# Performance work log

Hardware: AMD Instinct MI355X
Metric: run time of the kernel (lower is better)

The kernel has to match this reference:

```python
import jax, jax.numpy as jnp
import numpy as np

NUM_CLS = 80
C = 256
IMG = 1024.0
N = 256
SR = 2  # sampling_ratio
MIN_SIZE = 16.0
SCALES = (0.25, 0.125, 0.0625, 0.03125)
HW = ((256, 256), (128, 128), (64, 64), (32, 32))


def _roialign(feat, rois, scale, out):
    # feat: [C, H, W]; rois: [n, 4] (y1, x1, y2, x2) in image coords.
    # torchvision-style ROIAlign (aligned=False), sampling_ratio=SR, avg pool.
    Cc, H, W = feat.shape
    n = rois.shape[0]
    y1 = rois[:, 0] * scale
    x1 = rois[:, 1] * scale
    rh = jnp.maximum(rois[:, 2] * scale - y1, 1.0)
    rw = jnp.maximum(rois[:, 3] * scale - x1, 1.0)
    # per-bin sample offsets: (bin + (s+0.5)/SR) * bin_size
    g = (jnp.arange(out, dtype=feat.dtype)[:, None]
         + (jnp.arange(SR, dtype=feat.dtype)[None, :] + 0.5) / SR).reshape(-1)  # [out*SR]
    ys = y1[:, None] + g[None, :] * (rh / out)[:, None]  # [n, out*SR]
    xs = x1[:, None] + g[None, :] * (rw / out)[:, None]
    S = out * SR
    yy = jnp.broadcast_to(ys[:, :, None], (n, S, S)).reshape(n, S * S)
    xx = jnp.broadcast_to(xs[:, None, :], (n, S, S)).reshape(n, S * S)
    valid = (yy > -1.0) & (yy < H) & (xx > -1.0) & (xx < W)
    yc = jnp.clip(yy, 0.0, H - 1.0)
    xc = jnp.clip(xx, 0.0, W - 1.0)
    y0 = jnp.floor(yc)
    x0 = jnp.floor(xc)
    ly = yc - y0
    lx = xc - x0
    y0i = y0.astype(jnp.int32)
    x0i = x0.astype(jnp.int32)
    y1i = jnp.minimum(y0i + 1, H - 1)
    x1i = jnp.minimum(x0i + 1, W - 1)
    f00 = feat[:, y0i, x0i]  # [C, n, S*S]
    f01 = feat[:, y0i, x1i]
    f10 = feat[:, y1i, x0i]
    f11 = feat[:, y1i, x1i]
    val = (f00 * (1 - ly) * (1 - lx) + f01 * (1 - ly) * lx
           + f10 * ly * (1 - lx) + f11 * ly * lx)
    val = jnp.where(valid[None], val, 0.0)
    val = val.reshape(Cc, n, out, SR, out, SR).mean(axis=(3, 5))
    return val.transpose(1, 0, 2, 3)  # [n, C, out, out]


def _pool(P, rois, out):
    # roi_layer: FPN level assignment via log2 of sqrt(area)/224, clamp to levels 0..3
    area = jnp.prod(rois[:, 2:4] - rois[:, 0:2] + 1.0, axis=-1)
    lvl = jnp.clip(jnp.floor(4.0 + jnp.log(jnp.sqrt(area) / 224.0) / np.log(2.0)), 2.0, 5.0) - 2.0
    lvl = lvl.astype(jnp.int32)
    pooled = jnp.zeros((rois.shape[0], C, out, out), dtype=rois.dtype)
    for l in range(4):
        pl = _roialign(P[l], rois, SCALES[l], out)
        pooled = pooled + jnp.where((lvl == l)[:, None, None, None], pl, 0.0)
    return pooled


def _loc2bbox(loc, anchor):
    chw = anchor[..., 2:4] - anchor[..., 0:2]
    cyx = anchor[..., 0:2] + chw * 0.5
    yx = loc[..., 0:2] * chw + cyx
    hw = jnp.exp(loc[..., 2:4]) * chw
    return jnp.concatenate([yx - hw * 0.5, yx + hw * 0.5], axis=-1)


def _head(x, W1, b1, W2, b2, Wc, bc, Wl, bl):
    x = x.reshape(x.shape[0], -1)
    h = jax.nn.relu(x @ W1 + b1)
    h = jax.nn.relu(h @ W2 + b2)
    return h @ Wc + bc, h @ Wl + bl


def _cascade(P, rois, params):
    stds = (jnp.array([0.1, 0.1, 0.2, 0.2], dtype=rois.dtype),
            jnp.array([0.05, 0.05, 0.1, 0.1], dtype=rois.dtype),
            jnp.array([1 / 30.0, 1 / 30.0, 1 / 15.0, 1 / 15.0], dtype=rois.dtype))
    roi = rois
    valid = jnp.ones((rois.shape[0],), dtype=bool)
    t = jnp.arange(rois.shape[0])
    pre_b = jnp.zeros((rois.shape[0], NUM_CLS, 4), dtype=rois.dtype)
    pre_s = jnp.zeros((rois.shape[0], NUM_CLS), dtype=rois.dtype)
    for s in range(3):
        x = _pool(P, roi, 7)
        logits, loc = _head(x, *params[s])
        loc = loc.reshape(-1, NUM_CLS + 1, 4)[:, 1:] * stds[s]
        boxes = _loc2bbox(loc, roi[:, None, :])  # [N, NUM_CLS, 4]
        score = jax.nn.softmax(logits, axis=-1)[:, 1:]
        pre_b = pre_b + boxes
        pre_s = pre_s + score
        best = jnp.argmax(score, axis=-1)
        roi = boxes[t, best]
        roi = jnp.clip(roi, 0.0, IMG)  # square image: clamp both coords to [0, IMG]
        if s < 2:  # original filters only after stages 1 and 2
            hw = roi[:, 2:4] - roi[:, 0:2]
            valid = valid & jnp.all(hw >= MIN_SIZE, axis=-1)
    m = valid.astype(pre_s.dtype)
    return pre_b / 3.0 * m[:, None, None], pre_s / 3.0 * m[:, None]


def setup_inputs():
    key = jax.random.key(0)
    ks = jax.random.split(key, 32)
    inp = {}
    for i, (h, w) in enumerate(HW):
        inp[f"P{i}"] = jax.random.normal(ks[i], (C, h, w), dtype=jnp.float32)
    yx1 = jax.random.uniform(ks[4], (N, 2), minval=0.0, maxval=IMG - 64.0)
    sz = jnp.exp(jax.random.uniform(ks[5], (N, 2), minval=np.log(16.0), maxval=np.log(600.0)))
    yx2 = jnp.clip(yx1 + sz, 0.0, IMG - 1.0)
    inp["rois"] = jnp.concatenate([yx1, yx2], axis=-1).astype(jnp.float32)
    dims = [(C * 49, 1024), (1024,), (1024, 1024), (1024,),
            (1024, NUM_CLS + 1), (NUM_CLS + 1,), (1024, (NUM_CLS + 1) * 4), ((NUM_CLS + 1) * 4,)]
    names = ["W1", "b1", "W2", "b2", "Wc", "bc", "Wl", "bl"]
    k = 6
    for s in range(3):
        for nm, d in zip(names, dims):
            if len(d) == 1:
                inp[f"s{s}_{nm}"] = jnp.zeros(d, dtype=jnp.float32)
            else:
                inp[f"s{s}_{nm}"] = 0.02 * jax.random.normal(ks[k], d, dtype=jnp.float32)
                k += 1
    return inp


def reference(P0, P1, P2, P3, rois,
              s0_W1, s0_b1, s0_W2, s0_b2, s0_Wc, s0_bc, s0_Wl, s0_bl,
              s1_W1, s1_b1, s1_W2, s1_b2, s1_Wc, s1_bc, s1_Wl, s1_bl,
              s2_W1, s2_b1, s2_W2, s2_b2, s2_Wc, s2_bc, s2_Wl, s2_bl):
    P = (P0, P1, P2, P3)
    params = [(s0_W1, s0_b1, s0_W2, s0_b2, s0_Wc, s0_bc, s0_Wl, s0_bl),
              (s1_W1, s1_b1, s1_W2, s1_b2, s1_Wc, s1_bc, s1_Wl, s1_bl),
              (s2_W1, s2_b1, s2_W2, s2_b2, s2_Wc, s2_bc, s2_Wl, s2_bl)]
    return _cascade(P, rois, params)
```

## Files before the change

kernel.cpp:

```cpp
#include <hip/hip_runtime.h>
#include <math.h>


#define NROI 256
#define NCLS 80
#define APITCH 40

typedef __attribute__((ext_vector_type(8))) short short8;
typedef __attribute__((ext_vector_type(4))) float f32x4;

__device__ __forceinline__ unsigned short f2bf(float f) {
  unsigned u = __builtin_bit_cast(unsigned, f);
  unsigned r = (u + 0x7FFFu + ((u >> 16) & 1u)) >> 16;
  return (unsigned short)r;
}
__device__ __forceinline__ float bf2f(unsigned short u) {
  return __builtin_bit_cast(float, (unsigned)u << 16);
}

__global__ __launch_bounds__(256) void init_kernel(const float* __restrict__ rois,
                                                   float* __restrict__ roi,
                                                   float* __restrict__ valid) {
  int i = blockIdx.x * 256 + threadIdx.x;
  if (i < NROI * 4) roi[i] = rois[i];
  if (i < NROI) valid[i] = 1.0f;
}

__global__ __launch_bounds__(256) void transpose_bf16(const float* __restrict__ W,
                                                      unsigned short* __restrict__ Wt,
                                                      int K, int N) {
  __shared__ unsigned short tile[32][33];
  int t = threadIdx.x;
  int k0 = blockIdx.x * 32;
  int n0 = blockIdx.y * 32;
  int r = t >> 3;
  int c4 = (t & 7) * 4;
  float4 v = *(const float4*)(W + (size_t)(k0 + r) * N + n0 + c4);
  tile[r][c4 + 0] = f2bf(v.x);
  tile[r][c4 + 1] = f2bf(v.y);
  tile[r][c4 + 2] = f2bf(v.z);
  tile[r][c4 + 3] = f2bf(v.w);
  __syncthreads();
  struct __attribute__((aligned(8))) US4 { unsigned short a, b, c, d; } o;
  o.a = tile[c4 + 0][r];
  o.b = tile[c4 + 1][r];
  o.c = tile[c4 + 2][r];
  o.d = tile[c4 + 3][r];
  *(US4*)(Wt + (size_t)(n0 + r) * K + k0 + c4) = o;
}

__global__ __launch_bounds__(256) void transpose_w1(const float* __restrict__ W,
                                                    unsigned short* __restrict__ Wt) {
  __shared__ unsigned short tile[32][33];
  int t = threadIdx.x;
  int kd0 = blockIdx.x * 32;
  int n0 = blockIdx.y * 32;
  int p = kd0 >> 8;
  int c0 = kd0 & 255;
  int r = t >> 3;
  int c4 = (t & 7) * 4;
  int k_src = (c0 + r) * 49 + p;
  float4 v = *(const float4*)(W + (size_t)k_src * 1024 + n0 + c4);
  tile[r][c4 + 0] = f2bf(v.x);
  tile[r][c4 + 1] = f2bf(v.y);
  tile[r][c4 + 2] = f2bf(v.z);
  tile[r][c4 + 3] = f2bf(v.w);
  __syncthreads();
  struct __attribute__((aligned(8))) US4 { unsigned short a, b, c, d; } o;
  o.a = tile[c4 + 0][r];
  o.b = tile[c4 + 1][r];
  o.c = tile[c4 + 2][r];
  o.d = tile[c4 + 3][r];
  *(US4*)(Wt + (size_t)(n0 + r) * 12544 + kd0 + c4) = o;
}

__global__ __launch_bounds__(256) void head_transpose(const float* __restrict__ Wc,
                                                      const float* __restrict__ Wl,
                                                      unsigned short* __restrict__ Wt) {
  __shared__ unsigned short tile[32][33];
  int t = threadIdx.x;
  int k0 = blockIdx.x * 32;
  int n0 = blockIdx.y * 32;
  int r = t >> 3;
  int c4 = (t & 7) * 4;
#pragma unroll
  for (int j = 0; j < 4; j++) {
    int nn = n0 + c4 + j;
    float v = 0.0f;
    if (nn < 81) v = Wc[(size_t)(k0 + r) * 81 + nn];
    else if (nn < 405) v = Wl[(size_t)(k0 + r) * 324 + (nn - 81)];
    tile[r][c4 + j] = f2bf(v);
  }
  __syncthreads();
  struct __attribute__((aligned(8))) US4 { unsigned short a, b, c, d; } o;
  o.a = tile[c4 + 0][r];
  o.b = tile[c4 + 1][r];
  o.c = tile[c4 + 2][r];
  o.d = tile[c4 + 3][r];
  *(US4*)(Wt + (size_t)(n0 + r) * 1024 + k0 + c4) = o;
}

__global__ __launch_bounds__(256) void pool_kernel2(
    const unsigned short* __restrict__ Pb0, const unsigned short* __restrict__ Pb1,
    const unsigned short* __restrict__ Pb2, const unsigned short* __restrict__ Pb3,
    const float* __restrict__ roi, unsigned short* __restrict__ pooled) {
  int t = threadIdx.x;
  int n = blockIdx.y;
  int p = blockIdx.x * 4 + (t >> 6);
  if (p >= 49) return;
  int lane = t & 63;
  int c4 = lane * 4;
  int py = p / 7, px = p % 7;

  float r0 = roi[n * 4 + 0];
  float r1 = roi[n * 4 + 1];
  float r2 = roi[n * 4 + 2];
  float r3 = roi[n * 4 + 3];

  float area = (r2 - r0 + 1.0f) * (r3 - r1 + 1.0f);
  float lf = floorf(4.0f + log2f(sqrtf(area) / 224.0f));
  lf = fminf(fmaxf(lf, 2.0f), 5.0f);
  int lvl = (int)lf - 2;

  float scale;
  int H;
  const unsigned short* fb;
  if (lvl == 0)      { scale = 0.25f;    H = 256; fb = Pb0; }
  else if (lvl == 1) { scale = 0.125f;   H = 128; fb = Pb1; }
  else if (lvl == 2) { scale = 0.0625f;  H = 64;  fb = Pb2; }
  else               { scale = 0.03125f; H = 32;  fb = Pb3; }
  int W = H;

  float y1 = r0 * scale;
  float x1 = r1 * scale;
  float rh = fmaxf(r2 * scale - y1, 1.0f);
  float rw = fmaxf(r3 * scale - x1, 1.0f);
  float bh = rh * (1.0f / 7.0f);
  float bw = rw * (1.0f / 7.0f);

  float a0 = 0.f, a1 = 0.f, a2 = 0.f, a3 = 0.f;
#pragma unroll
  for (int ry = 0; ry < 2; ry++) {
    float yy = y1 + ((float)py + ((float)ry + 0.5f) * 0.5f) * bh;
    bool vy = (yy > -1.0f) && (yy < (float)H);
    float ycl = fminf(fmaxf(yy, 0.0f), (float)(H - 1));
    float y0f = floorf(ycl);
    float ly = ycl - y0f;
    int y0i = (int)y0f;
    int y1i = min(y0i + 1, H - 1);
#pragma unroll
    for (int rx = 0; rx < 2; rx++) {
      float xx = x1 + ((float)px + ((float)rx + 0.5f) * 0.5f) * bw;
      bool vx = (xx > -1.0f) && (xx < (float)W);
      float xcl = fminf(fmaxf(xx, 0.0f), (float)(W - 1));
      float x0f = floorf(xcl);
      float lx = xcl - x0f;
      int x0i = (int)x0f;
      int x1i = min(x0i + 1, W - 1);
      float w00 = (1.f - ly) * (1.f - lx);
      float w01 = (1.f - ly) * lx;
      float w10 = ly * (1.f - lx);
      float w11 = ly * lx;
      if (!(vy && vx)) { w00 = w01 = w10 = w11 = 0.f; }
      ushort4 f00 = *(const ushort4*)(fb + ((size_t)(y0i * W + x0i) * 256 + c4));
      ushort4 f01 = *(const ushort4*)(fb + ((size_t)(y0i * W + x1i) * 256 + c4));
      ushort4 f10 = *(const ushort4*)(fb + ((size_t)(y1i * W + x0i) * 256 + c4));
      ushort4 f11 = *(const ushort4*)(fb + ((size_t)(y1i * W + x1i) * 256 + c4));
      a0 += bf2f(f00.x) * w00 + bf2f(f01.x) * w01 + bf2f(f10.x) * w10 + bf2f(f11.x) * w11;
      a1 += bf2f(f00.y) * w00 + bf2f(f01.y) * w01 + bf2f(f10.y) * w10 + bf2f(f11.y) * w11;
      a2 += bf2f(f00.z) * w00 + bf2f(f01.z) * w01 + bf2f(f10.z) * w10 + bf2f(f11.z) * w11;
      a3 += bf2f(f00.w) * w00 + bf2f(f01.w) * w01 + bf2f(f10.w) * w10 + bf2f(f11.w) * w11;
    }
  }
  ushort4 o;
  o.x = f2bf(a0 * 0.25f);
  o.y = f2bf(a1 * 0.25f);
  o.z = f2bf(a2 * 0.25f);
  o.w = f2bf(a3 * 0.25f);
  *(ushort4*)(pooled + (size_t)n * 12544 + p * 256 + c4) = o;
}

__global__ __launch_bounds__(256) void gemm_bf16(
    const unsigned short* __restrict__ A, const unsigned short* __restrict__ B,
    float* __restrict__ Cpart, int M, int N, int K, int iters) {
  __shared__ unsigned short As[128 * APITCH];
  __shared__ unsigned short Bs[128 * APITCH];
  const int t = threadIdx.x;
  const int n0 = blockIdx.x * 128;
  const int m0 = blockIdx.y * 128;
  const size_t kt0 = (size_t)blockIdx.z * iters * 32;

  const int row = t >> 2;
  const int off = (t & 3) * 8;
  const unsigned short* pa0 = A + (size_t)(m0 + row) * K + kt0 + off;
  const unsigned short* pa1 = pa0 + (size_t)64 * K;
  const unsigned short* pb0 = B + (size_t)(n0 + row) * K + kt0 + off;
  const unsigned short* pb1 = pb0 + (size_t)64 * K;

  const int lane = t & 63;
  const int wave = t >> 6;
  const int wm = (wave >> 1) * 64;
  const int wn = (wave & 1) * 64;
  const int fr = lane & 15;
  const int kq = (lane >> 4) * 8;

  f32x4 acc[4][4];
#pragma unroll
  for (int i = 0; i < 4; i++)
#pragma unroll
    for (int j = 0; j < 4; j++) acc[i][j] = (f32x4){0.f, 0.f, 0.f, 0.f};

  uint4 ra0 = *(const uint4*)pa0;
  uint4 ra1 = *(const uint4*)pa1;
  uint4 rb0 = *(const uint4*)pb0;
  uint4 rb1 = *(const uint4*)pb1;

  for (int it = 0; it < iters; ++it) {
    *(uint4*)&As[row * APITCH + off] = ra0;
    *(uint4*)&As[(row + 64) * APITCH + off] = ra1;
    *(uint4*)&Bs[row * APITCH + off] = rb0;
    *(uint4*)&Bs[(row + 64) * APITCH + off] = rb1;
    __syncthreads();
    if (it + 1 < iters) {
      int d = (it + 1) * 32;
      ra0 = *(const uint4*)(pa0 + d);
      ra1 = *(const uint4*)(pa1 + d);
      rb0 = *(const uint4*)(pb0 + d);
      rb1 = *(const uint4*)(pb1 + d);
    }
    short8 af[4], bfv[4];
#pragma unroll
    for (int f = 0; f < 4; f++)
      af[f] = *(const short8*)&As[(wm + f * 16 + fr) * APITCH + kq];
#pragma unroll
    for (int f = 0; f < 4; f++)
      bfv[f] = *(const short8*)&Bs[(wn + f * 16 + fr) * APITCH + kq];
#pragma unroll
    for (int fm = 0; fm < 4; fm++)
#pragma unroll
      for (int fn = 0; fn < 4; fn++)
        acc[fm][fn] = __builtin_amdgcn_mfma_f32_16x16x32_bf16(af[fm], bfv[fn],
                                                              acc[fm][fn], 0, 0, 0);
    __syncthreads();
  }

  float* Cp = Cpart + (size_t)blockIdx.z * M * N;
  const int colb = n0 + wn + fr;
  const int rowb = m0 + wm + (lane >> 4) * 4;
#pragma unroll
  for (int fm = 0; fm < 4; fm++)
#pragma unroll
    for (int fn = 0; fn < 4; fn++)
#pragma unroll
      for (int r = 0; r < 4; r++)
        Cp[(size_t)(rowb + fm * 16 + r) * N + (colb + fn * 16)] = acc[fm][fn][r];
}

__global__ __launch_bounds__(256) void reduce_bias_relu(
    const float* __restrict__ parts, int nparts, const float* __restrict__ bias,
    unsigned short* __restrict__ outb) {
  int i = blockIdx.x * 256 + threadIdx.x;
  float s = 0.0f;
  for (int p = 0; p < nparts; ++p) s += parts[(size_t)p * 262144 + i];
  s = fmaxf(s + bias[i & 1023], 0.0f);
  outb[i] = f2bf(s);
}

__global__ __launch_bounds__(128) void decode_kernel(
    const float* __restrict__ headp, const float* __restrict__ bc,
    const float* __restrict__ bl,
    float* __restrict__ roi, float* __restrict__ valid,
    float* __restrict__ pre_b, float* __restrict__ pre_s,
    float st0, float st1, float st2, float st3, int stage) {
  int n = blockIdx.x;
  int t = threadIdx.x;
  __shared__ float red[128];
  __shared__ int redi[128];
  __shared__ float sroi[4];
  __shared__ float boxes[NCLS][4];

  if (t < 4) sroi[t] = roi[n * 4 + t];
  float l = -INFINITY;
  if (t < 81) {
    float s = 0.f;
#pragma unroll
    for (int z = 0; z < 4; z++) s += headp[(size_t)z * 131072 + n * 512 + t];
    l = s + bc[t];
  }
  red[t] = l;
  __syncthreads();
#pragma unroll
  for (int s = 64; s > 0; s >>= 1) {
    if (t < s) red[t] = fmaxf(red[t], red[t + s]);
    __syncthreads();
  }
  float mx = red[0];
  __syncthreads();
  red[t] = (t < 81) ? expf(l - mx) : 0.0f;
  __syncthreads();
#pragma unroll
  for (int s = 64; s > 0; s >>= 1) {
    if (t < s) red[t] += red[t + s];
    __syncthreads();
  }
  float denom = red[0];
  __syncthreads();

  float score = -INFINITY;
  if (t < NCLS) {
    float lj = 0.f;
#pragma unroll
    for (int z = 0; z < 4; z++) lj += headp[(size_t)z * 131072 + n * 512 + (t + 1)];
    lj += bc[t + 1];
    score = expf(lj - mx) / denom;
    float lp[4];
#pragma unroll
    for (int j = 0; j < 4; j++) {
      float s = 0.f;
#pragma unroll
      for (int z = 0; z < 4; z++)
        s += headp[(size_t)z * 131072 + n * 512 + 81 + (t + 1) * 4 + j];
      lp[j] = s + bl[(t + 1) * 4 + j];
    }
    float dy = lp[0] * st0;
    float dx = lp[1] * st1;
    float dh = lp[2] * st2;
    float dw = lp[3] * st3;
    float h_ = sroi[2] - sroi[0];
    float w_ = sroi[3] - sroi[1];
    float cy = sroi[0] + h_ * 0.5f;
    float cx = sroi[1] + w_ * 0.5f;
    float ny = dy * h_ + cy;
    float nx = dx * w_ + cx;
    float nh = expf(dh) * h_;
    float nw = expf(dw) * w_;
    float b0 = ny - nh * 0.5f;
    float b1v = nx - nw * 0.5f;
    float b2v = ny + nh * 0.5f;
    float b3v = nx + nw * 0.5f;
    int o = (n * NCLS + t) * 4;
    pre_b[o + 0] += b0;
    pre_b[o + 1] += b1v;
    pre_b[o + 2] += b2v;
    pre_b[o + 3] += b3v;
    pre_s[n * NCLS + t] += score;
    boxes[t][0] = b0;
    boxes[t][1] = b1v;
    boxes[t][2] = b2v;
    boxes[t][3] = b3v;
  }
  red[t] = score;
  redi[t] = t;
  __syncthreads();
  for (int s = 64; s > 0; s >>= 1) {
    if (t < s) {
      float o2 = red[t + s];
      int oi = redi[t + s];
      if (o2 > red[t] || (o2 == red[t] && oi < redi[t])) {
        red[t] = o2;
        redi[t] = oi;
      }
    }
    __syncthreads();
  }
  if (t == 0) {
    int best = redi[0];
    float ry1 = fminf(fmaxf(boxes[best][0], 0.0f), 1024.0f);
    float rx1 = fminf(fmaxf(boxes[best][1], 0.0f), 1024.0f);
    float ry2 = fminf(fmaxf(boxes[best][2], 0.0f), 1024.0f);
    float rx2 = fminf(fmaxf(boxes[best][3], 0.0f), 1024.0f);
    roi[n * 4 + 0] = ry1;
    roi[n * 4 + 1] = rx1;
    roi[n * 4 + 2] = ry2;
    roi[n * 4 + 3] = rx2;
    if (stage < 2) {
      float hh = ry2 - ry1, ww = rx2 - rx1;
      if (!(hh >= 16.0f && ww >= 16.0f)) valid[n] = 0.0f;
    }
  }
}

__global__ __launch_bounds__(256) void finalize_kernel(
    const float* __restrict__ pre_b, const float* __restrict__ pre_s,
    const float* __restrict__ valid, float* __restrict__ out) {
  int i = blockIdx.x * 256 + threadIdx.x;
  if (i < NROI * NCLS * 4) {
    int n = i / (NCLS * 4);
    out[i] = pre_b[i] * valid[n] * (1.0f / 3.0f);
  } else if (i < NROI * NCLS * 4 + NROI * NCLS) {
    int j = i - NROI * NCLS * 4;
    int n = j / NCLS;
    out[i] = pre_s[j] * valid[n] * (1.0f / 3.0f);
  }
}

extern "C" void kernel_launch(void* const* d_in, const int* in_sizes, int n_in,
                              void* d_out, int out_size, void* d_ws, size_t ws_size,
                              hipStream_t stream) {
  const float* P0 = (const float*)d_in[0];
  const float* P1 = (const float*)d_in[1];
  const float* P2 = (const float*)d_in[2];
  const float* P3 = (const float*)d_in[3];
  const float* rois = (const float*)d_in[4];
  float* out = (float*)d_out;
  float* ws = (float*)d_ws;

  float* roi   = ws;
  float* valid = roi + 1024;
  float* pre_b = valid + 256;
  float* pre_s = pre_b + 81920;
  float* part1 = pre_s + 20480;
  float* part2 = part1 + 14 * 262144;
  float* parth = part2 + 8 * 262144;
  unsigned short* pooledb = (unsigned short*)(parth + 4 * 131072);
  unsigned short* Wt1 = pooledb + (size_t)256 * 12544;
  unsigned short* Wt2 = Wt1 + (size_t)1024 * 12544;
  unsigned short* Wth = Wt2 + (size_t)1024 * 1024;
  unsigned short* h1b = Wth + (size_t)512 * 1024;
  unsigned short* h2b = h1b + (size_t)256 * 1024;
  unsigned short* Pb0 = h2b + (size_t)256 * 1024;
  unsigned short* Pb1 = Pb0 + (size_t)65536 * 256;
  unsigned short* Pb2 = Pb1 + (size_t)16384 * 256;
  unsigned short* Pb3 = Pb2 + (size_t)4096 * 256;

  init_kernel<<<4, 256, 0, stream>>>(rois, roi, valid);
  hipMemsetAsync(pre_b, 0, (size_t)(81920 + 20480) * sizeof(float), stream);

  transpose_bf16<<<dim3(8, 2048), 256, 0, stream>>>(P0, Pb0, 256, 65536);
  transpose_bf16<<<dim3(8, 512),  256, 0, stream>>>(P1, Pb1, 256, 16384);
  transpose_bf16<<<dim3(8, 128),  256, 0, stream>>>(P2, Pb2, 256, 4096);
  transpose_bf16<<<dim3(8, 32),   256, 0, stream>>>(P3, Pb3, 256, 1024);

  const float stds[3][4] = {
      {0.1f, 0.1f, 0.2f, 0.2f},
      {0.05f, 0.05f, 0.1f, 0.1f},
      {1.0f / 30.0f, 1.0f / 30.0f, 1.0f / 15.0f, 1.0f / 15.0f}};

  for (int s = 0; s < 3; s++) {
    const float* W1 = (const float*)d_in[5 + s * 8 + 0];
    const float* b1 = (const float*)d_in[5 + s * 8 + 1];
    const float* W2 = (const float*)d_in[5 + s * 8 + 2];
    const float* b2 = (const float*)d_in[5 + s * 8 + 3];
    const float* Wc = (const float*)d_in[5 + s * 8 + 4];
    const float* bc = (const float*)d_in[5 + s * 8 + 5];
    const float* Wl = (const float*)d_in[5 + s * 8 + 6];
    const float* bl = (const float*)d_in[5 + s * 8 + 7];

    transpose_w1<<<dim3(392, 32), 256, 0, stream>>>(W1, Wt1);
    transpose_bf16<<<dim3(32, 32), 256, 0, stream>>>(W2, Wt2, 1024, 1024);
    head_transpose<<<dim3(32, 16), 256, 0, stream>>>(Wc, Wl, Wth);

    pool_kernel2<<<dim3(13, 256), 256, 0, stream>>>(Pb0, Pb1, Pb2, Pb3, roi, pooledb);

    gemm_bf16<<<dim3(8, 2, 14), 256, 0, stream>>>(pooledb, Wt1, part1, 256, 1024, 12544, 28);
    reduce_bias_relu<<<1024, 256, 0, stream>>>(part1, 14, b1, h1b);

    gemm_bf16<<<dim3(8, 2, 8), 256, 0, stream>>>(h1b, Wt2, part2, 256, 1024, 1024, 4);
    reduce_bias_relu<<<1024, 256, 0, stream>>>(part2, 8, b2, h2b);

    gemm_bf16<<<dim3(4, 2, 4), 256, 0, stream>>>(h2b, Wth, parth, 256, 512, 1024, 8);

    decode_kernel<<<256, 128, 0, stream>>>(parth, bc, bl, roi, valid, pre_b, pre_s,
                                           stds[s][0], stds[s][1], stds[s][2], stds[s][3], s);
  }

  finalize_kernel<<<400, 256, 0, stream>>>(pre_b, pre_s, valid, out);
}
```

Baseline: 499.5 us.

## Merge all feature and weight conversions into one prep launch, fold init/finalize into decode

```diff
diff --git a/kernel.cpp b/kernel.cpp
--- a/kernel.cpp
+++ b/kernel.cpp
@@ -18,24 +18,85 @@
   return __builtin_bit_cast(float, (unsigned)u << 16);
 }
 
-__global__ __launch_bounds__(256) void init_kernel(const float* __restrict__ rois,
-                                                   float* __restrict__ roi,
-                                                   float* __restrict__ valid) {
-  int i = blockIdx.x * 256 + threadIdx.x;
-  if (i < NROI * 4) roi[i] = rois[i];
-  if (i < NROI) valid[i] = 1.0f;
-}
-
-__global__ __launch_bounds__(256) void transpose_bf16(const float* __restrict__ W,
-                                                      unsigned short* __restrict__ Wt,
-                                                      int K, int N) {
+__global__ __launch_bounds__(256) void prep_kernel(
+    const float* __restrict__ P0, const float* __restrict__ P1,
+    const float* __restrict__ P2, const float* __restrict__ P3,
+    unsigned short* __restrict__ Pb0, unsigned short* __restrict__ Pb1,
+    unsigned short* __restrict__ Pb2, unsigned short* __restrict__ Pb3,
+    const float* __restrict__ W1a, const float* __restrict__ W1b,
+    const float* __restrict__ W1c,
+    const float* __restrict__ W2a, const float* __restrict__ W2b,
+    const float* __restrict__ W2c,
+    const float* __restrict__ Wca, const float* __restrict__ Wcb,
+    const float* __restrict__ Wcc,
+    const float* __restrict__ Wla, const float* __restrict__ Wlb,
+    const float* __restrict__ Wlc,
+    unsigned short* __restrict__ Wt1, unsigned short* __restrict__ Wt2,
+    unsigned short* __restrict__ Wth) {
   __shared__ unsigned short tile[32][33];
+  int bid = blockIdx.x;
   int t = threadIdx.x;
-  int k0 = blockIdx.x * 32;
-  int n0 = blockIdx.y * 32;
   int r = t >> 3;
   int c4 = (t & 7) * 4;
-  float4 v = *(const float4*)(W + (size_t)(k0 + r) * N + n0 + c4);
+
+  float4 v;
+  unsigned short* dptr;
+
+  if (bid < 21760) {
+    const float* S;
+    unsigned short* D;
+    int N, idx;
+    if (bid < 16384)      { S = P0; D = Pb0; N = 65536; idx = bid; }
+    else if (bid < 20480) { S = P1; D = Pb1; N = 16384; idx = bid - 16384; }
+    else if (bid < 21504) { S = P2; D = Pb2; N = 4096;  idx = bid - 20480; }
+    else                  { S = P3; D = Pb3; N = 1024;  idx = bid - 21504; }
+    int k0 = (idx & 7) * 32;
+    int n0 = (idx >> 3) * 32;
+    v = *(const float4*)(S + (size_t)(k0 + r) * N + n0 + c4);
+    dptr = D + (size_t)(n0 + r) * 256 + k0 + c4;
+  } else if (bid < 59392) {
+    int idx = bid - 21760;
+    int s = idx / 12544;
+    idx -= s * 12544;
+    const float* W = (s == 0) ? W1a : (s == 1) ? W1b : W1c;
+    int bx = idx % 392;
+    int by = idx / 392;
+    int kd0 = bx * 32;
+    int n0 = by * 32;
+    int p = kd0 >> 8;
+    int c0 = kd0 & 255;
+    v = *(const float4*)(W + (size_t)((c0 + r) * 49 + p) * 1024 + n0 + c4);
+    dptr = Wt1 + (size_t)s * 12544 * 1024 + (size_t)(n0 + r) * 12544 + kd0 + c4;
+  } else if (bid < 62464) {
+    int idx = bid - 59392;
+    int s = idx >> 10;
+    idx &= 1023;
+    const float* W = (s == 0) ? W2a : (s == 1) ? W2b : W2c;
+    int k0 = (idx & 31) * 32;
+    int n0 = (idx >> 5) * 32;
+    v = *(const float4*)(W + (size_t)(k0 + r) * 1024 + n0 + c4);
+    dptr = Wt2 + (size_t)s * 1024 * 1024 + (size_t)(n0 + r) * 1024 + k0 + c4;
+  } else {
+    int idx = bid - 62464;
+    int s = idx >> 9;
+    idx &= 511;
+    const float* wc = (s == 0) ? Wca : (s == 1) ? Wcb : Wcc;
+    const float* wl = (s == 0) ? Wla : (s == 1) ? Wlb : Wlc;
+    int k0 = (idx & 31) * 32;
+    int n0 = (idx >> 5) * 32;
+    float vv[4];
+#pragma unroll
+    for (int j = 0; j < 4; j++) {
+      int nn = n0 + c4 + j;
+      float x = 0.0f;
+      if (nn < 81) x = wc[(size_t)(k0 + r) * 81 + nn];
+      else if (nn < 405) x = wl[(size_t)(k0 + r) * 324 + (nn - 81)];
+      vv[j] = x;
+    }
+    v.x = vv[0]; v.y = vv[1]; v.z = vv[2]; v.w = vv[3];
+    dptr = Wth + (size_t)s * 512 * 1024 + (size_t)(n0 + r) * 1024 + k0 + c4;
+  }
+
   tile[r][c4 + 0] = f2bf(v.x);
   tile[r][c4 + 1] = f2bf(v.y);
   tile[r][c4 + 2] = f2bf(v.z);
@@ -46,58 +107,7 @@
   o.b = tile[c4 + 1][r];
   o.c = tile[c4 + 2][r];
   o.d = tile[c4 + 3][r];
-  *(US4*)(Wt + (size_t)(n0 + r) * K + k0 + c4) = o;
-}
-
-__global__ __launch_bounds__(256) void transpose_w1(const float* __restrict__ W,
-                                                    unsigned short* __restrict__ Wt) {
-  __shared__ unsigned short tile[32][33];
-  int t = threadIdx.x;
-  int kd0 = blockIdx.x * 32;
-  int n0 = blockIdx.y * 32;
-  int p = kd0 >> 8;
-  int c0 = kd0 & 255;
-  int r = t >> 3;
-  int c4 = (t & 7) * 4;
-  int k_src = (c0 + r) * 49 + p;
-  float4 v = *(const float4*)(W + (size_t)k_src * 1024 + n0 + c4);
-  tile[r][c4 + 0] = f2bf(v.x);
-  tile[r][c4 + 1] = f2bf(v.y);
-  tile[r][c4 + 2] = f2bf(v.z);
-  tile[r][c4 + 3] = f2bf(v.w);
-  __syncthreads();
-  struct __attribute__((aligned(8))) US4 { unsigned short a, b, c, d; } o;
-  o.a = tile[c4 + 0][r];
-  o.b = tile[c4 + 1][r];
-  o.c = tile[c4 + 2][r];
-  o.d = tile[c4 + 3][r];
-  *(US4*)(Wt + (size_t)(n0 + r) * 12544 + kd0 + c4) = o;
-}
-
-__global__ __launch_bounds__(256) void head_transpose(const float* __restrict__ Wc,
-                                                      const float* __restrict__ Wl,
-                                                      unsigned short* __restrict__ Wt) {
-  __shared__ unsigned short tile[32][33];
-  int t = threadIdx.x;
-  int k0 = blockIdx.x * 32;
-  int n0 = blockIdx.y * 32;
-  int r = t >> 3;
-  int c4 = (t & 7) * 4;
-#pragma unroll
-  for (int j = 0; j < 4; j++) {
-    int nn = n0 + c4 + j;
-    float v = 0.0f;
-    if (nn < 81) v = Wc[(size_t)(k0 + r) * 81 + nn];
-    else if (nn < 405) v = Wl[(size_t)(k0 + r) * 324 + (nn - 81)];
-    tile[r][c4 + j] = f2bf(v);
-  }
-  __syncthreads();
-  struct __attribute__((aligned(8))) US4 { unsigned short a, b, c, d; } o;
-  o.a = tile[c4 + 0][r];
-  o.b = tile[c4 + 1][r];
-  o.c = tile[c4 + 2][r];
-  o.d = tile[c4 + 3][r];
-  *(US4*)(Wt + (size_t)(n0 + r) * 1024 + k0 + c4) = o;
+  *(US4*)dptr = o;
 }
 
 __global__ __launch_bounds__(256) void pool_kernel2(
@@ -269,8 +279,10 @@
 __global__ __launch_bounds__(128) void decode_kernel(
     const float* __restrict__ headp, const float* __restrict__ bc,
     const float* __restrict__ bl,
-    float* __restrict__ roi, float* __restrict__ valid,
+    const float* __restrict__ roi_in, float* __restrict__ roi_out,
+    float* __restrict__ valid,
     float* __restrict__ pre_b, float* __restrict__ pre_s,
+    float* __restrict__ out,
     float st0, float st1, float st2, float st3, int stage) {
   int n = blockIdx.x;
   int t = threadIdx.x;
@@ -279,7 +291,7 @@
   __shared__ float sroi[4];
   __shared__ float boxes[NCLS][4];
 
-  if (t < 4) sroi[t] = roi[n * 4 + t];
+  if (t < 4) sroi[t] = roi_in[n * 4 + t];
   float l = -INFINITY;
   if (t < 81) {
     float s = 0.f;
@@ -339,58 +351,63 @@
     float b2v = ny + nh * 0.5f;
     float b3v = nx + nw * 0.5f;
     int o = (n * NCLS + t) * 4;
-    pre_b[o + 0] += b0;
-    pre_b[o + 1] += b1v;
-    pre_b[o + 2] += b2v;
-    pre_b[o + 3] += b3v;
-    pre_s[n * NCLS + t] += score;
-    boxes[t][0] = b0;
-    boxes[t][1] = b1v;
-    boxes[t][2] = b2v;
-    boxes[t][3] = b3v;
-  }
-  red[t] = score;
-  redi[t] = t;
-  __syncthreads();
-  for (int s = 64; s > 0; s >>= 1) {
-    if (t < s) {
-      float o2 = red[t + s];
-      int oi = redi[t + s];
-      if (o2 > red[t] || (o2 == red[t] && oi < redi[t])) {
-        red[t] = o2;
-        redi[t] = oi;
+    if (stage == 0) {
+      pre_b[o + 0] = b0;
+      pre_b[o + 1] = b1v;
+      pre_b[o + 2] = b2v;
+      pre_b[o + 3] = b3v;
+      pre_s[n * NCLS + t] = score;
+    } else if (stage == 1) {
+      pre_b[o + 0] += b0;
+      pre_b[o + 1] += b1v;
+      pre_b[o + 2] += b2v;
+      pre_b[o + 3] += b3v;
+      pre_s[n * NCLS + t] += score;
+    } else {
+      float vm = valid[n] * (1.0f / 3.0f);
+      out[o + 0] = (pre_b[o + 0] + b0) * vm;
+      out[o + 1] = (pre_b[o + 1] + b1v) * vm;
+      out[o + 2] = (pre_b[o + 2] + b2v) * vm;
+      out[o + 3] = (pre_b[o + 3] + b3v) * vm;
+      out[NROI * NCLS * 4 + n * NCLS + t] = (pre_s[n * NCLS + t] + score) * vm;
+    }
+    if (stage < 2) {
+      boxes[t][0] = b0;
+      boxes[t][1] = b1v;
+      boxes[t][2] = b2v;
+      boxes[t][3] = b3v;
+    }
+  }
+  if (stage < 2) {
+    red[t] = score;
+    redi[t] = t;
+    __syncthreads();
+    for (int s = 64; s > 0; s >>= 1) {
+      if (t < s) {
+        float o2 = red[t + s];
+        int oi = redi[t + s];
+        if (o2 > red[t] || (o2 == red[t] && oi < redi[t])) {
+          red[t] = o2;
+          redi[t] = oi;
+        }
       }
-    }
-    __syncthreads();
-  }
-  if (t == 0) {
-    int best = redi[0];
-    float ry1 = fminf(fmaxf(boxes[best][0], 0.0f), 1024.0f);
-    float rx1 = fminf(fmaxf(boxes[best][1], 0.0f), 1024.0f);
-    float ry2 = fminf(fmaxf(boxes[best][2], 0.0f), 1024.0f);
-    float rx2 = fminf(fmaxf(boxes[best][3], 0.0f), 1024.0f);
-    roi[n * 4 + 0] = ry1;
-    roi[n * 4 + 1] = rx1;
-    roi[n * 4 + 2] = ry2;
-    roi[n * 4 + 3] = rx2;
-    if (stage < 2) {
+      __syncthreads();
+    }
+    if (t == 0) {
+      int best = redi[0];
+      float ry1 = fminf(fmaxf(boxes[best][0], 0.0f), 1024.0f);
+      float rx1 = fminf(fmaxf(boxes[best][1], 0.0f), 1024.0f);
+      float ry2 = fminf(fmaxf(boxes[best][2], 0.0f), 1024.0f);
+      float rx2 = fminf(fmaxf(boxes[best][3], 0.0f), 1024.0f);
+      roi_out[n * 4 + 0] = ry1;
+      roi_out[n * 4 + 1] = rx1;
+      roi_out[n * 4 + 2] = ry2;
+      roi_out[n * 4 + 3] = rx2;
       float hh = ry2 - ry1, ww = rx2 - rx1;
-      if (!(hh >= 16.0f && ww >= 16.0f)) valid[n] = 0.0f;
-    }
-  }
-}
-
-__global__ __launch_bounds__(256) void finalize_kernel(
-    const float* __restrict__ pre_b, const float* __restrict__ pre_s,
-    const float* __restrict__ valid, float* __restrict__ out) {
-  int i = blockIdx.x * 256 + threadIdx.x;
-  if (i < NROI * NCLS * 4) {
-    int n = i / (NCLS * 4);
-    out[i] = pre_b[i] * valid[n] * (1.0f / 3.0f);
-  } else if (i < NROI * NCLS * 4 + NROI * NCLS) {
-    int j = i - NROI * NCLS * 4;
-    int n = j / NCLS;
-    out[i] = pre_s[j] * valid[n] * (1.0f / 3.0f);
+      bool ok = (hh >= 16.0f && ww >= 16.0f);
+      if (stage == 0) valid[n] = ok ? 1.0f : 0.0f;
+      else if (!ok) valid[n] = 0.0f;
+    }
   }
 }
 
@@ -410,26 +427,30 @@
   float* pre_b = valid + 256;
   float* pre_s = pre_b + 81920;
   float* part1 = pre_s + 20480;
-  float* part2 = part1 + 14 * 262144;
-  float* parth = part2 + 8 * 262144;
-  unsigned short* pooledb = (unsigned short*)(parth + 4 * 131072);
+  float* part2 = part1 + (size_t)14 * 262144;
+  float* parth = part2 + (size_t)8 * 262144;
+  unsigned short* pooledb = (unsigned short*)(parth + (size_t)4 * 131072);
   unsigned short* Wt1 = pooledb + (size_t)256 * 12544;
-  unsigned short* Wt2 = Wt1 + (size_t)1024 * 12544;
-  unsigned short* Wth = Wt2 + (size_t)1024 * 1024;
-  unsigned short* h1b = Wth + (size_t)512 * 1024;
+  unsigned short* Wt2 = Wt1 + (size_t)3 * 12544 * 1024;
+  unsigned short* Wth = Wt2 + (size_t)3 * 1024 * 1024;
+  unsigned short* h1b = Wth + (size_t)3 * 512 * 1024;
   unsigned short* h2b = h1b + (size_t)256 * 1024;
   unsigned short* Pb0 = h2b + (size_t)256 * 1024;
   unsigned short* Pb1 = Pb0 + (size_t)65536 * 256;
   unsigned short* Pb2 = Pb1 + (size_t)16384 * 256;
   unsigned short* Pb3 = Pb2 + (size_t)4096 * 256;
 
-  init_kernel<<<4, 256, 0, stream>>>(rois, roi, valid);
-  hipMemsetAsync(pre_b, 0, (size_t)(81920 + 20480) * sizeof(float), stream);
-
-  transpose_bf16<<<dim3(8, 2048), 256, 0, stream>>>(P0, Pb0, 256, 65536);
-  transpose_bf16<<<dim3(8, 512),  256, 0, stream>>>(P1, Pb1, 256, 16384);
-  transpose_bf16<<<dim3(8, 128),  256, 0, stream>>>(P2, Pb2, 256, 4096);
-  transpose_bf16<<<dim3(8, 32),   256, 0, stream>>>(P3, Pb3, 256, 1024);
+  prep_kernel<<<64000, 256, 0, stream>>>(
+      P0, P1, P2, P3, Pb0, Pb1, Pb2, Pb3,
+      (const float*)d_in[5 + 0 * 8 + 0], (const float*)d_in[5 + 1 * 8 + 0],
+      (const float*)d_in[5 + 2 * 8 + 0],
+      (const float*)d_in[5 + 0 * 8 + 2], (const float*)d_in[5 + 1 * 8 + 2],
+      (const float*)d_in[5 + 2 * 8 + 2],
+      (const float*)d_in[5 + 0 * 8 + 4], (const float*)d_in[5 + 1 * 8 + 4],
+      (const float*)d_in[5 + 2 * 8 + 4],
+      (const float*)d_in[5 + 0 * 8 + 6], (const float*)d_in[5 + 1 * 8 + 6],
+      (const float*)d_in[5 + 2 * 8 + 6],
+      Wt1, Wt2, Wth);
 
   const float stds[3][4] = {
       {0.1f, 0.1f, 0.2f, 0.2f},
@@ -437,32 +458,28 @@
       {1.0f / 30.0f, 1.0f / 30.0f, 1.0f / 15.0f, 1.0f / 15.0f}};
 
   for (int s = 0; s < 3; s++) {
-    const float* W1 = (const float*)d_in[5 + s * 8 + 0];
     const float* b1 = (const float*)d_in[5 + s * 8 + 1];
-    const float* W2 = (const float*)d_in[5 + s * 8 + 2];
     const float* b2 = (const float*)d_in[5 + s * 8 + 3];
-    const float* Wc = (const float*)d_in[5 + s * 8 + 4];
     const float* bc = (const float*)d_in[5 + s * 8 + 5];
-    const float* Wl = (const float*)d_in[5 + s * 8 + 6];
     const float* bl = (const float*)d_in[5 + s * 8 + 7];
-
-    transpose_w1<<<dim3(392, 32), 256, 0, stream>>>(W1, Wt1);
-    transpose_bf16<<<dim3(32, 32), 256, 0, stream>>>(W2, Wt2, 1024, 1024);
-    head_transpose<<<dim3(32, 16), 256, 0, stream>>>(Wc, Wl, Wth);
-
-    pool_kernel2<<<dim3(13, 256), 256, 0, stream>>>(Pb0, Pb1, Pb2, Pb3, roi, pooledb);
-
-    gemm_bf16<<<dim3(8, 2, 14), 256, 0, stream>>>(pooledb, Wt1, part1, 256, 1024, 12544, 28);
+    const float* roi_src = (s == 0) ? rois : roi;
+
+    pool_kernel2<<<dim3(13, 256), 256, 0, stream>>>(Pb0, Pb1, Pb2, Pb3, roi_src,
+                                                    pooledb);
+
+    gemm_bf16<<<dim3(8, 2, 14), 256, 0, stream>>>(
+        pooledb, Wt1 + (size_t)s * 12544 * 1024, part1, 256, 1024, 12544, 28);
     reduce_bias_relu<<<1024, 256, 0, stream>>>(part1, 14, b1, h1b);
 
-    gemm_bf16<<<dim3(8, 2, 8), 256, 0, stream>>>(h1b, Wt2, part2, 256, 1024, 1024, 4);
+    gemm_bf16<<<dim3(8, 2, 8), 256, 0, stream>>>(
+        h1b, Wt2 + (size_t)s * 1024 * 1024, part2, 256, 1024, 1024, 4);
     reduce_bias_relu<<<1024, 256, 0, stream>>>(part2, 8, b2, h2b);
 
-    gemm_bf16<<<dim3(4, 2, 4), 256, 0, stream>>>(h2b, Wth, parth, 256, 512, 1024, 8);
-
-    decode_kernel<<<256, 128, 0, stream>>>(parth, bc, bl, roi, valid, pre_b, pre_s,
-                                           stds[s][0], stds[s][1], stds[s][2], stds[s][3], s);
-  }
-
-  finalize_kernel<<<400, 256, 0, stream>>>(pre_b, pre_s, valid, out);
-}
+    gemm_bf16<<<dim3(4, 2, 4), 256, 0, stream>>>(
+        h2b, Wth + (size_t)s * 512 * 1024, parth, 256, 512, 1024, 8);
+
+    decode_kernel<<<256, 128, 0, stream>>>(parth, bc, bl, roi_src, roi, valid,
+                                           pre_b, pre_s, out, stds[s][0],
+                                           stds[s][1], stds[s][2], stds[s][3], s);
+  }
+}
```

Result: faster. 481.3 us (-3.6%).
